# Kernel optimization log

Hardware: AMD Instinct MI355X
Metric: run time of the kernel (lower is better)

Reference implementation:

```python
import math
import jax, jax.numpy as jnp
import numpy as np

B, H, HW, C = 4, 8, 2048, 64
TEMPERATURE = 8.0  # sqrt(head_dim)
EPS = 0.5


def _l2norm(x, axis):
    return x / (1e-6 + jnp.linalg.norm(x, axis=axis, keepdims=True))


def setup_inputs() -> dict:
    key = jax.random.key(0)
    kq, kk, kv, ka = jax.random.split(key, 4)
    q = jax.random.normal(kq, (B, H, HW, C), dtype=jnp.float32)
    k = jax.random.normal(kk, (B, H, HW, C), dtype=jnp.float32)
    v = jax.random.normal(kv, (B, H, HW, C), dtype=jnp.float32)
    a_rand = jax.random.normal(ka, (B, H, HW, C), dtype=jnp.float32) * math.sqrt(2.0 / C)
    return {"q": q, "k": k, "v": v, "a_rand": a_rand}


def reference(q, k, v, a_rand):
    # Elementwise OT-style score modification of K
    k_l2 = _l2norm(k, -1)
    v_l2 = _l2norm(v, -1)
    kv_sim = jnp.clip(k_l2 * v_l2, 0.0, None)        # [B,H,HW,C]
    K_mat = jnp.exp(-(1.0 - kv_sim) / EPS)
    a = _l2norm(a_rand, 1)                            # normalize over heads dim
    b = k / K_mat * a
    a2 = v / K_mat * b
    k_updated = k * a2
    # Full N^2 attention with modified keys
    attn = jax.nn.softmax(
        jnp.einsum('bhqc,bhkc->bhqk', q / TEMPERATURE, k_updated), axis=-1
    )                                                 # [B,H,HW,HW]
    out = jnp.einsum('bhqk,bhkc->bhqc', attn, v)      # [B,H,HW,C]
    return out, attn
```

## Files before the change

kernel.cpp:

```cpp
#include <hip/hip_runtime.h>
#include <hip/hip_bf16.h>
#include <math.h>

#define B_ 4
#define H_ 8
#define N_ 2048
#define C_ 64
#define BM 64
#define BN 64
#define LDH 72

typedef _Float16 half8 __attribute__((ext_vector_type(8)));
typedef _Float16 half4 __attribute__((ext_vector_type(4)));
typedef float f32x4 __attribute__((ext_vector_type(4)));

#if __has_builtin(__builtin_amdgcn_exp2f)
#define EXP2(x) __builtin_amdgcn_exp2f(x)
#else
#define EXP2(x) exp2f(x)
#endif

__global__ __launch_bounds__(512) void prep_kernel(
    const float* __restrict__ k,
    const float* __restrict__ v,
    const float* __restrict__ a_rand,
    _Float16* __restrict__ kup_hi,
    _Float16* __restrict__ kup_lo)
{
    int bn = blockIdx.x;
    int b = bn >> 11, n = bn & (N_ - 1);
    int t = threadIdx.x;
    int h = t >> 6, c = t & 63;
    size_t idx = (((size_t)(b * H_ + h)) * N_ + n) * C_ + c;
    float kf = k[idx];
    float vf = v[idx];
    float af = a_rand[idx];
    float ks = kf * kf, vs = vf * vf;
    #pragma unroll
    for (int m = 1; m < 64; m <<= 1) {
        ks += __shfl_xor(ks, m, 64);
        vs += __shfl_xor(vs, m, 64);
    }
    float kinv = 1.0f / (1e-6f + sqrtf(ks));
    float vinv = 1.0f / (1e-6f + sqrtf(vs));
    __shared__ float a2s[H_][C_];
    a2s[h][c] = af * af;
    __syncthreads();
    float asum = 0.0f;
    #pragma unroll
    for (int hh = 0; hh < H_; hh++) asum += a2s[hh][c];
    float ainv = 1.0f / (1e-6f + sqrtf(asum));
    float s = fmaxf(kf * kinv * vf * vinv, 0.0f);
    float kupf = kf * kf * vf * (af * ainv) * EXP2(5.7707801635558535f * (1.0f - s));
    kupf = fminf(fmaxf(kupf, -60000.0f), 60000.0f);
    _Float16 hi = (_Float16)kupf;
    _Float16 lo = (_Float16)(kupf - (float)hi);
    kup_hi[idx] = hi;
    kup_lo[idx] = lo;
}

__global__ __launch_bounds__(256) void attn_kernel(
    const float* __restrict__ q,
    const float* __restrict__ v,
    const _Float16* __restrict__ kup_hi,
    const _Float16* __restrict__ kup_lo,
    float* __restrict__ out,
    float* __restrict__ attn)
{
    __shared__ __align__(16) _Float16 Qs[BM * LDH];
    __shared__ __align__(16) _Float16 Ql[BM * LDH];
    __shared__ __align__(16) _Float16 Ks[BN * LDH];
    __shared__ __align__(16) _Float16 Kl[BN * LDH];
    __shared__ __align__(16) _Float16 Vt[C_ * LDH];
    __shared__ __align__(16) _Float16 Ps[BM * LDH];

    int bh = blockIdx.x;
    int qb = blockIdx.y * BM;
    int t = threadIdx.x;
    int w = t >> 6, lane = t & 63;
    int quad = lane >> 4, lc = lane & 15;

    const size_t base = (size_t)bh * N_ * C_;
    const float* qg = q + base + (size_t)qb * C_;
    const _Float16* kgh = kup_hi + base;
    const _Float16* kgl = kup_lo + base;
    const float* vg = v + base;

    const float qscale = 0.18033688011112042f;
    #pragma unroll
    for (int it = 0; it < 4; it++) {
        int idx = it * 256 + t;
        int row = idx >> 4, seg = idx & 15;
        float4 d = *(const float4*)(qg + (size_t)row * C_ + seg * 4);
        float f0 = d.x * qscale, f1 = d.y * qscale, f2 = d.z * qscale, f3 = d.w * qscale;
        half4 hv, lv;
        hv[0] = (_Float16)f0; lv[0] = (_Float16)(f0 - (float)hv[0]);
        hv[1] = (_Float16)f1; lv[1] = (_Float16)(f1 - (float)hv[1]);
        hv[2] = (_Float16)f2; lv[2] = (_Float16)(f2 - (float)hv[2]);
        hv[3] = (_Float16)f3; lv[3] = (_Float16)(f3 - (float)hv[3]);
        *(half4*)&Qs[row * LDH + seg * 4] = hv;
        *(half4*)&Ql[row * LDH + seg * 4] = lv;
    }
    __syncthreads();

    half8 qa0 = *(half8*)&Qs[(w * 16 + lc) * LDH + 0 + quad * 8];
    half8 qa1 = *(half8*)&Qs[(w * 16 + lc) * LDH + 32 + quad * 8];
    half8 ql0 = *(half8*)&Ql[(w * 16 + lc) * LDH + 0 + quad * 8];
    half8 ql1 = *(half8*)&Ql[(w * 16 + lc) * LDH + 32 + quad * 8];

    float m_run[4], l_run[4];
    f32x4 Oacc[4];
    #pragma unroll
    for (int r = 0; r < 4; r++) { m_run[r] = -INFINITY; l_run[r] = 0.0f; }
    #pragma unroll
    for (int sc = 0; sc < 4; sc++) Oacc[sc] = (f32x4){0.f, 0.f, 0.f, 0.f};

    for (int j0 = 0; j0 < N_; j0 += BN) {
        __syncthreads();
        #pragma unroll
        for (int it = 0; it < 2; it++) {
            int idx = it * 256 + t;
            int row = idx >> 3, seg = idx & 7;
            *(half8*)&Ks[row * LDH + seg * 8] =
                *(const half8*)(kgh + (size_t)(j0 + row) * C_ + seg * 8);
            *(half8*)&Kl[row * LDH + seg * 8] =
                *(const half8*)(kgl + (size_t)(j0 + row) * C_ + seg * 8);
        }
        __syncthreads();
        f32x4 S[4];
        #pragma unroll
        for (int s = 0; s < 4; s++) {
            half8 bh0 = *(half8*)&Ks[(s * 16 + lc) * LDH + 0 + quad * 8];
            half8 bh1 = *(half8*)&Ks[(s * 16 + lc) * LDH + 32 + quad * 8];
            half8 bl0 = *(half8*)&Kl[(s * 16 + lc) * LDH + 0 + quad * 8];
            half8 bl1 = *(half8*)&Kl[(s * 16 + lc) * LDH + 32 + quad * 8];
            f32x4 acc = (f32x4){0.f, 0.f, 0.f, 0.f};
            acc = __builtin_amdgcn_mfma_f32_16x16x32_f16(qa0, bh0, acc, 0, 0, 0);
            acc = __builtin_amdgcn_mfma_f32_16x16x32_f16(qa1, bh1, acc, 0, 0, 0);
            acc = __builtin_amdgcn_mfma_f32_16x16x32_f16(qa0, bl0, acc, 0, 0, 0);
            acc = __builtin_amdgcn_mfma_f32_16x16x32_f16(qa1, bl1, acc, 0, 0, 0);
            acc = __builtin_amdgcn_mfma_f32_16x16x32_f16(ql0, bh0, acc, 0, 0, 0);
            acc = __builtin_amdgcn_mfma_f32_16x16x32_f16(ql1, bh1, acc, 0, 0, 0);
            S[s] = acc;
        }
        #pragma unroll
        for (int r = 0; r < 4; r++) {
            float mloc = fmaxf(fmaxf(S[0][r], S[1][r]), fmaxf(S[2][r], S[3][r]));
            #pragma unroll
            for (int msk = 1; msk < 16; msk <<= 1)
                mloc = fmaxf(mloc, __shfl_xor(mloc, msk, 64));
            float mnew = fmaxf(m_run[r], mloc);
            float rs = EXP2(S[0][r] - mnew) + EXP2(S[1][r] - mnew) +
                       EXP2(S[2][r] - mnew) + EXP2(S[3][r] - mnew);
            #pragma unroll
            for (int msk = 1; msk < 16; msk <<= 1)
                rs += __shfl_xor(rs, msk, 64);
            l_run[r] = l_run[r] * EXP2(m_run[r] - mnew) + rs;
            m_run[r] = mnew;
        }
    }
    float linv[4];
    #pragma unroll
    for (int r = 0; r < 4; r++) linv[r] = 1.0f / l_run[r];

    float* attng = attn + (size_t)bh * N_ * N_ + (size_t)qb * N_;

    for (int j0 = 0; j0 < N_; j0 += BN) {
        __syncthreads();
        #pragma unroll
        for (int it = 0; it < 2; it++) {
            int idx = it * 256 + t;
            int row = idx >> 3, seg = idx & 7;
            *(half8*)&Ks[row * LDH + seg * 8] =
                *(const half8*)(kgh + (size_t)(j0 + row) * C_ + seg * 8);
            *(half8*)&Kl[row * LDH + seg * 8] =
                *(const half8*)(kgl + (size_t)(j0 + row) * C_ + seg * 8);
        }
        {
            int key = t >> 2, cb = (t & 3) * 16;
            const float* vr = vg + (size_t)(j0 + key) * C_ + cb;
            #pragma unroll
            for (int i = 0; i < 16; i += 4) {
                float4 d = *(const float4*)(vr + i);
                Vt[(cb + i + 0) * LDH + key] = (_Float16)d.x;
                Vt[(cb + i + 1) * LDH + key] = (_Float16)d.y;
                Vt[(cb + i + 2) * LDH + key] = (_Float16)d.z;
                Vt[(cb + i + 3) * LDH + key] = (_Float16)d.w;
            }
        }
        __syncthreads();
        f32x4 S[4];
        #pragma unroll
        for (int s = 0; s < 4; s++) {
            half8 bh0 = *(half8*)&Ks[(s * 16 + lc) * LDH + 0 + quad * 8];
            half8 bh1 = *(half8*)&Ks[(s * 16 + lc) * LDH + 32 + quad * 8];
            half8 bl0 = *(half8*)&Kl[(s * 16 + lc) * LDH + 0 + quad * 8];
            half8 bl1 = *(half8*)&Kl[(s * 16 + lc) * LDH + 32 + quad * 8];
            f32x4 acc = (f32x4){0.f, 0.f, 0.f, 0.f};
            acc = __builtin_amdgcn_mfma_f32_16x16x32_f16(qa0, bh0, acc, 0, 0, 0);
            acc = __builtin_amdgcn_mfma_f32_16x16x32_f16(qa1, bh1, acc, 0, 0, 0);
            acc = __builtin_amdgcn_mfma_f32_16x16x32_f16(qa0, bl0, acc, 0, 0, 0);
            acc = __builtin_amdgcn_mfma_f32_16x16x32_f16(qa1, bl1, acc, 0, 0, 0);
            acc = __builtin_amdgcn_mfma_f32_16x16x32_f16(ql0, bh0, acc, 0, 0, 0);
            acc = __builtin_amdgcn_mfma_f32_16x16x32_f16(ql1, bh1, acc, 0, 0, 0);
            S[s] = acc;
        }
        #pragma unroll
        for (int s = 0; s < 4; s++) {
            #pragma unroll
            for (int r = 0; r < 4; r++) {
                float p = EXP2(S[s][r] - m_run[r]) * linv[r];
                Ps[(w * 16 + quad * 4 + r) * LDH + s * 16 + lc] = (_Float16)p;
            }
        }
        __syncthreads();
        #pragma unroll
        for (int kn = 0; kn < 2; kn++) {
            half8 pa = *(half8*)&Ps[(w * 16 + lc) * LDH + kn * 32 + quad * 8];
            #pragma unroll
            for (int sc = 0; sc < 4; sc++) {
                half8 vb = *(half8*)&Vt[(sc * 16 + lc) * LDH + kn * 32 + quad * 8];
                Oacc[sc] = __builtin_amdgcn_mfma_f32_16x16x32_f16(pa, vb, Oacc[sc], 0, 0, 0);
            }
        }
        #pragma unroll
        for (int it = 0; it < 4; it++) {
            int idx = it * 256 + t;
            int row = idx >> 4, seg = idx & 15;
            half4 hv = *(half4*)&Ps[row * LDH + seg * 4];
            float4 o;
            o.x = (float)hv[0];
            o.y = (float)hv[1];
            o.z = (float)hv[2];
            o.w = (float)hv[3];
            *(float4*)(attng + (size_t)row * N_ + j0 + seg * 4) = o;
        }
    }

    float* og = out + base + (size_t)qb * C_;
    #pragma unroll
    for (int sc = 0; sc < 4; sc++) {
        #pragma unroll
        for (int r = 0; r < 4; r++) {
            og[(size_t)(w * 16 + quad * 4 + r) * C_ + sc * 16 + lc] = Oacc[sc][r];
        }
    }
}

extern "C" void kernel_launch(void* const* d_in, const int* in_sizes, int n_in,
                              void* d_out, int out_size, void* d_ws, size_t ws_size,
                              hipStream_t stream) {
    const float* q = (const float*)d_in[0];
    const float* k = (const float*)d_in[1];
    const float* v = (const float*)d_in[2];
    const float* a = (const float*)d_in[3];
    const size_t nelem = (size_t)B_ * H_ * N_ * C_;
    _Float16* kup_hi = (_Float16*)d_ws;
    _Float16* kup_lo = kup_hi + nelem;
    float* out = (float*)d_out;
    float* attn = out + nelem;

    prep_kernel<<<dim3(B_ * N_), dim3(512), 0, stream>>>(k, v, a, kup_hi, kup_lo);
    attn_kernel<<<dim3(B_ * H_, N_ / BM), dim3(256), 0, stream>>>(q, v, kup_hi, kup_lo, out, attn);
}
```

Measured before the change: 782.8 us.

## Defer softmax row reductions, alias Q/K smem, skew V transpose layout

The first pass now keeps per-lane running max/sum statistics and merges them across the 16 lanes once at the end with a log-sum-exp combine, instead of doing cross-lane shuffles every tile. The Q staging buffers are reused for K tiles, and the occupancy hint is raised to 4 blocks per CU. This frees shared memory for more resident blocks. The transposed V tile gets a per-column-group offset to reduce LDS bank conflicts. Register pressure under the tighter launch bound could cause spills.

```diff
diff --git a/kernel.cpp b/kernel.cpp
--- a/kernel.cpp
+++ b/kernel.cpp
@@ -59,7 +59,7 @@
     kup_lo[idx] = lo;
 }
 
-__global__ __launch_bounds__(256) void attn_kernel(
+__global__ __launch_bounds__(256, 4) void attn_kernel(
     const float* __restrict__ q,
     const float* __restrict__ v,
     const _Float16* __restrict__ kup_hi,
@@ -67,11 +67,9 @@
     float* __restrict__ out,
     float* __restrict__ attn)
 {
-    __shared__ __align__(16) _Float16 Qs[BM * LDH];
-    __shared__ __align__(16) _Float16 Ql[BM * LDH];
-    __shared__ __align__(16) _Float16 Ks[BN * LDH];
-    __shared__ __align__(16) _Float16 Kl[BN * LDH];
-    __shared__ __align__(16) _Float16 Vt[C_ * LDH];
+    __shared__ __align__(16) _Float16 KQh[BM * LDH];
+    __shared__ __align__(16) _Float16 KQl[BM * LDH];
+    __shared__ __align__(16) _Float16 Vt[C_ * LDH + 64];
     __shared__ __align__(16) _Float16 Ps[BM * LDH];
 
     int bh = blockIdx.x;
@@ -98,15 +96,15 @@
         hv[1] = (_Float16)f1; lv[1] = (_Float16)(f1 - (float)hv[1]);
         hv[2] = (_Float16)f2; lv[2] = (_Float16)(f2 - (float)hv[2]);
         hv[3] = (_Float16)f3; lv[3] = (_Float16)(f3 - (float)hv[3]);
-        *(half4*)&Qs[row * LDH + seg * 4] = hv;
-        *(half4*)&Ql[row * LDH + seg * 4] = lv;
+        *(half4*)&KQh[row * LDH + seg * 4] = hv;
+        *(half4*)&KQl[row * LDH + seg * 4] = lv;
     }
     __syncthreads();
 
-    half8 qa0 = *(half8*)&Qs[(w * 16 + lc) * LDH + 0 + quad * 8];
-    half8 qa1 = *(half8*)&Qs[(w * 16 + lc) * LDH + 32 + quad * 8];
-    half8 ql0 = *(half8*)&Ql[(w * 16 + lc) * LDH + 0 + quad * 8];
-    half8 ql1 = *(half8*)&Ql[(w * 16 + lc) * LDH + 32 + quad * 8];
+    half8 qa0 = *(half8*)&KQh[(w * 16 + lc) * LDH + 0 + quad * 8];
+    half8 qa1 = *(half8*)&KQh[(w * 16 + lc) * LDH + 32 + quad * 8];
+    half8 ql0 = *(half8*)&KQl[(w * 16 + lc) * LDH + 0 + quad * 8];
+    half8 ql1 = *(half8*)&KQl[(w * 16 + lc) * LDH + 32 + quad * 8];
 
     float m_run[4], l_run[4];
     f32x4 Oacc[4];
@@ -121,19 +119,19 @@
         for (int it = 0; it < 2; it++) {
             int idx = it * 256 + t;
             int row = idx >> 3, seg = idx & 7;
-            *(half8*)&Ks[row * LDH + seg * 8] =
+            *(half8*)&KQh[row * LDH + seg * 8] =
                 *(const half8*)(kgh + (size_t)(j0 + row) * C_ + seg * 8);
-            *(half8*)&Kl[row * LDH + seg * 8] =
+            *(half8*)&KQl[row * LDH + seg * 8] =
                 *(const half8*)(kgl + (size_t)(j0 + row) * C_ + seg * 8);
         }
         __syncthreads();
         f32x4 S[4];
         #pragma unroll
         for (int s = 0; s < 4; s++) {
-            half8 bh0 = *(half8*)&Ks[(s * 16 + lc) * LDH + 0 + quad * 8];
-            half8 bh1 = *(half8*)&Ks[(s * 16 + lc) * LDH + 32 + quad * 8];
-            half8 bl0 = *(half8*)&Kl[(s * 16 + lc) * LDH + 0 + quad * 8];
-            half8 bl1 = *(half8*)&Kl[(s * 16 + lc) * LDH + 32 + quad * 8];
+            half8 bh0 = *(half8*)&KQh[(s * 16 + lc) * LDH + 0 + quad * 8];
+            half8 bh1 = *(half8*)&KQh[(s * 16 + lc) * LDH + 32 + quad * 8];
+            half8 bl0 = *(half8*)&KQl[(s * 16 + lc) * LDH + 0 + quad * 8];
+            half8 bl1 = *(half8*)&KQl[(s * 16 + lc) * LDH + 32 + quad * 8];
             f32x4 acc = (f32x4){0.f, 0.f, 0.f, 0.f};
             acc = __builtin_amdgcn_mfma_f32_16x16x32_f16(qa0, bh0, acc, 0, 0, 0);
             acc = __builtin_amdgcn_mfma_f32_16x16x32_f16(qa1, bh1, acc, 0, 0, 0);
@@ -146,22 +144,27 @@
         #pragma unroll
         for (int r = 0; r < 4; r++) {
             float mloc = fmaxf(fmaxf(S[0][r], S[1][r]), fmaxf(S[2][r], S[3][r]));
-            #pragma unroll
-            for (int msk = 1; msk < 16; msk <<= 1)
-                mloc = fmaxf(mloc, __shfl_xor(mloc, msk, 64));
             float mnew = fmaxf(m_run[r], mloc);
             float rs = EXP2(S[0][r] - mnew) + EXP2(S[1][r] - mnew) +
                        EXP2(S[2][r] - mnew) + EXP2(S[3][r] - mnew);
-            #pragma unroll
-            for (int msk = 1; msk < 16; msk <<= 1)
-                rs += __shfl_xor(rs, msk, 64);
             l_run[r] = l_run[r] * EXP2(m_run[r] - mnew) + rs;
             m_run[r] = mnew;
         }
     }
-    float linv[4];
-    #pragma unroll
-    for (int r = 0; r < 4; r++) linv[r] = 1.0f / l_run[r];
+    #pragma unroll
+    for (int r = 0; r < 4; r++) {
+        float m = m_run[r], l = l_run[r];
+        #pragma unroll
+        for (int msk = 1; msk < 16; msk <<= 1) {
+            float mo = __shfl_xor(m, msk, 64);
+            float lo = __shfl_xor(l, msk, 64);
+            float mn = fmaxf(m, mo);
+            l = l * EXP2(m - mn) + lo * EXP2(mo - mn);
+            m = mn;
+        }
+        m_run[r] = m;
+        l_run[r] = 1.0f / l;
+    }
 
     float* attng = attn + (size_t)bh * N_ * N_ + (size_t)qb * N_;
 
@@ -171,31 +174,32 @@
         for (int it = 0; it < 2; it++) {
             int idx = it * 256 + t;
             int row = idx >> 3, seg = idx & 7;
-            *(half8*)&Ks[row * LDH + seg * 8] =
+            *(half8*)&KQh[row * LDH + seg * 8] =
                 *(const half8*)(kgh + (size_t)(j0 + row) * C_ + seg * 8);
-            *(half8*)&Kl[row * LDH + seg * 8] =
+            *(half8*)&KQl[row * LDH + seg * 8] =
                 *(const half8*)(kgl + (size_t)(j0 + row) * C_ + seg * 8);
         }
         {
             int key = t >> 2, cb = (t & 3) * 16;
+            int ofs = (t & 3) * 16;
             const float* vr = vg + (size_t)(j0 + key) * C_ + cb;
             #pragma unroll
             for (int i = 0; i < 16; i += 4) {
                 float4 d = *(const float4*)(vr + i);
-                Vt[(cb + i + 0) * LDH + key] = (_Float16)d.x;
-                Vt[(cb + i + 1) * LDH + key] = (_Float16)d.y;
-                Vt[(cb + i + 2) * LDH + key] = (_Float16)d.z;
-                Vt[(cb + i + 3) * LDH + key] = (_Float16)d.w;
+                Vt[(cb + i + 0) * LDH + ofs + key] = (_Float16)d.x;
+                Vt[(cb + i + 1) * LDH + ofs + key] = (_Float16)d.y;
+                Vt[(cb + i + 2) * LDH + ofs + key] = (_Float16)d.z;
+                Vt[(cb + i + 3) * LDH + ofs + key] = (_Float16)d.w;
             }
         }
         __syncthreads();
         f32x4 S[4];
         #pragma unroll
         for (int s = 0; s < 4; s++) {
-            half8 bh0 = *(half8*)&Ks[(s * 16 + lc) * LDH + 0 + quad * 8];
-            half8 bh1 = *(half8*)&Ks[(s * 16 + lc) * LDH + 32 + quad * 8];
-            half8 bl0 = *(half8*)&Kl[(s * 16 + lc) * LDH + 0 + quad * 8];
-            half8 bl1 = *(half8*)&Kl[(s * 16 + lc) * LDH + 32 + quad * 8];
+            half8 bh0 = *(half8*)&KQh[(s * 16 + lc) * LDH + 0 + quad * 8];
+            half8 bh1 = *(half8*)&KQh[(s * 16 + lc) * LDH + 32 + quad * 8];
+            half8 bl0 = *(half8*)&KQl[(s * 16 + lc) * LDH + 0 + quad * 8];
+            half8 bl1 = *(half8*)&KQl[(s * 16 + lc) * LDH + 32 + quad * 8];
             f32x4 acc = (f32x4){0.f, 0.f, 0.f, 0.f};
             acc = __builtin_amdgcn_mfma_f32_16x16x32_f16(qa0, bh0, acc, 0, 0, 0);
             acc = __builtin_amdgcn_mfma_f32_16x16x32_f16(qa1, bh1, acc, 0, 0, 0);
@@ -209,7 +213,7 @@
         for (int s = 0; s < 4; s++) {
             #pragma unroll
             for (int r = 0; r < 4; r++) {
-                float p = EXP2(S[s][r] - m_run[r]) * linv[r];
+                float p = EXP2(S[s][r] - m_run[r]) * l_run[r];
                 Ps[(w * 16 + quad * 4 + r) * LDH + s * 16 + lc] = (_Float16)p;
             }
         }
@@ -219,7 +223,7 @@
             half8 pa = *(half8*)&Ps[(w * 16 + lc) * LDH + kn * 32 + quad * 8];
             #pragma unroll
             for (int sc = 0; sc < 4; sc++) {
-                half8 vb = *(half8*)&Vt[(sc * 16 + lc) * LDH + kn * 32 + quad * 8];
+                half8 vb = *(half8*)&Vt[(sc * 16 + lc) * LDH + sc * 16 + kn * 32 + quad * 8];
                 Oacc[sc] = __builtin_amdgcn_mfma_f32_16x16x32_f16(pa, vb, Oacc[sc], 0, 0, 0);
             }
         }
```

New measurement: 749.5 us. -4.3%, faster.
